# Performance work log

Hardware: AMD Instinct MI355X
Metric: run time of the kernel (lower is better)

Reference implementation:

```python
import jax, jax.numpy as jnp
import numpy as np

B, S, D, K = 8, 4096, 256, 8192
BETA = 0.25


def setup_inputs() -> dict:
    key = jax.random.key(0)
    k1, k2 = jax.random.split(key)
    return {
        "z": jax.random.normal(k1, (B, S, D), dtype=jnp.float32),
        "embed": jax.random.normal(k2, (K, D), dtype=jnp.float32),
    }


def reference(z, embed):
    # Inference-path VQ-EMA forward (EMA buffer updates are a no-grad side
    # effect only active in training mode; excluded from the pure reference).
    num_codes, dim = embed.shape
    z_flat = z.reshape(-1, dim)                      # [N, D]
    # squared-euclidean distances: ||z||^2 - 2 z.e^T + ||e||^2  -> [N, K]
    dist = ((z_flat * z_flat).sum(1, keepdims=True)
            - 2.0 * (z_flat @ embed.T)
            + (embed * embed).sum(1)[None, :])
    idx = jnp.argmin(dist, axis=1)                   # [N]
    z_q = embed[idx].reshape(z.shape)                # gather instead of onehot @ embed
    # commitment loss: beta * mse(stop_grad(z_q), z)
    loss = BETA * jnp.mean(jnp.square(jax.lax.stop_gradient(z_q) - z))
    # straight-through estimator
    z_q_st = z + jax.lax.stop_gradient(z_q - z)
    # perplexity from code usage histogram (scatter-add instead of onehot.mean)
    counts = jnp.zeros((num_codes,), dtype=z.dtype).at[idx].add(1.0)
    avg_probs = counts / idx.shape[0]
    perplexity = jnp.exp(-jnp.sum(avg_probs * jnp.log(avg_probs + 1e-12)))
    return z_q_st, loss, perplexity, idx.reshape(z.shape[:-1])
```

## Files before the change

kernel.cpp:

```cpp
#include <hip/hip_runtime.h>
#include <stdint.h>
#include <math.h>

#define NROWS 32768
#define DIM   256
#define KCODES 8192
#define BETA  0.25f
#define RSPLIT 16
#define NELEM 8388608
#define TAU 0.09375f

typedef float f32x4 __attribute__((ext_vector_type(4)));
typedef _Float16 v8h __attribute__((ext_vector_type(8)));
typedef unsigned short us4 __attribute__((ext_vector_type(4)));

__device__ inline unsigned int split1(float x) {
    _Float16 hf = (_Float16)x;
    _Float16 lf = (_Float16)(x - (float)hf);
    unsigned int h = __builtin_bit_cast(unsigned short, hf);
    unsigned int l = __builtin_bit_cast(unsigned short, lf);
    return h | (l << 16);
}

__device__ inline void gload_lds16(const void* g, void* l) {
    __builtin_amdgcn_global_load_lds(
        (const __attribute__((address_space(1))) void*)g,
        (__attribute__((address_space(3))) void*)l,
        16, 0, 0);
}

__device__ inline unsigned int fkey(float f) {
    unsigned int b = __float_as_uint(f);
    return (b & 0x80000000u) ? ~b : (b | 0x80000000u);
}

__global__ void prep_all(const float* __restrict__ z,
                         const float* __restrict__ e,
                         unsigned short* __restrict__ zhi,
                         unsigned short* __restrict__ zlo,
                         unsigned short* __restrict__ ehi,
                         unsigned short* __restrict__ elo,
                         float* __restrict__ enrm,
                         float* __restrict__ counts,
                         float* __restrict__ lossAcc,
                         int* __restrict__ flagcnt) {
    if (blockIdx.x < 8192) {
        int t = blockIdx.x * 256 + threadIdx.x;
        float4 v = reinterpret_cast<const float4*>(z)[t];
        unsigned int p0 = split1(v.x);
        unsigned int p1 = split1(v.y);
        unsigned int p2 = split1(v.z);
        unsigned int p3 = split1(v.w);
        us4 h, l;
        h[0] = (unsigned short)p0; l[0] = (unsigned short)(p0 >> 16);
        h[1] = (unsigned short)p1; l[1] = (unsigned short)(p1 >> 16);
        h[2] = (unsigned short)p2; l[2] = (unsigned short)(p2 >> 16);
        h[3] = (unsigned short)p3; l[3] = (unsigned short)(p3 >> 16);
        reinterpret_cast<us4*>(zhi)[t] = h;
        reinterpret_cast<us4*>(zlo)[t] = l;
    } else {
        int row = blockIdx.x - 8192;
        int d = threadIdx.x;
        float x = e[(size_t)row * DIM + d];
        unsigned int p = split1(x);
        ehi[(size_t)row * DIM + d] = (unsigned short)p;
        elo[(size_t)row * DIM + d] = (unsigned short)(p >> 16);
        float sq = x * x;
        #pragma unroll
        for (int off = 32; off; off >>= 1) sq += __shfl_down(sq, off);
        __shared__ float ps[4];
        if ((threadIdx.x & 63) == 0) ps[threadIdx.x >> 6] = sq;
        __syncthreads();
        if (threadIdx.x == 0) {
            enrm[row] = 0.5f * (ps[0] + ps[1] + ps[2] + ps[3]);
            counts[row] = 0.f;
            if (row == 0) { *lossAcc = 0.f; *flagcnt = 0; }
        }
    }
}

__launch_bounds__(512, 2)
__global__ void gemm_hi_fused(const unsigned short* __restrict__ zhi,
                              const unsigned short* __restrict__ ehi,
                              const float* __restrict__ enrm,
                              int* __restrict__ colidx,
                              float* __restrict__ out_idx,
                              int* __restrict__ flagcnt,
                              int* __restrict__ flaglist,
                              unsigned long long* __restrict__ rkey) {
    __shared__ __align__(16) unsigned short Bs[4][128 * 64];
    __shared__ float esL[KCODES];
    __shared__ float rvv[4][128];
    __shared__ float rv2s[4][128];
    __shared__ int   rcc[4][128];

    const int tid = threadIdx.x;
    const int w = tid >> 6, l = tid & 63;
    const int lx = l & 15, quad = l >> 4;
    const int wm = w >> 2, wn = w & 3;
    const int arow_base = blockIdx.x * 128;
    const int fr_lx7 = lx & 15 & 7;
    const int ecol = wn * 32 + lx;
    const int st_g = ((l & 7) ^ (l >> 3)) * 8;

    v8h af[4][8];
    #pragma unroll
    for (int mi = 0; mi < 4; ++mi) {
        const unsigned short* ap =
            zhi + (size_t)(arow_base + wm * 64 + mi * 16 + lx) * DIM + quad * 8;
        #pragma unroll
        for (int ks = 0; ks < 8; ++ks)
            af[mi][ks] = *(const v8h*)(ap + ks * 32);
    }

    #pragma unroll
    for (int j = 0; j < 4; ++j)
        gload_lds16(enrm + (j * 8 + w) * 256 + l * 4, &esL[(j * 8 + w) * 256]);

#define STAGE(BUF, NT, BK) do {                                               \
        const unsigned short* _s = ehi                                        \
            + (size_t)((NT) * 128 + (tid >> 3)) * DIM + (BK) * 64 + st_g;     \
        gload_lds16(_s,                    &Bs[BUF][(w * 8) * 64]);           \
        gload_lds16(_s + (size_t)64 * DIM, &Bs[BUF][(64 + w * 8) * 64]);      \
} while (0)

#define READF(DST, BUF) do {                                                  \
        _Pragma("unroll") for (int kc = 0; kc < 2; ++kc) {                    \
            const int gsw = ((kc * 4 + quad) ^ fr_lx7) * 8;                   \
            DST[kc * 2 + 0] = *(const v8h*)&Bs[BUF][(wn * 32 + lx) * 64 + gsw];      \
            DST[kc * 2 + 1] = *(const v8h*)&Bs[BUF][(wn * 32 + 16 + lx) * 64 + gsw]; \
        }                                                                     \
} while (0)

#define MFMAS(F, BK) do {                                                     \
        __builtin_amdgcn_s_setprio(1);                                        \
        _Pragma("unroll") for (int kc = 0; kc < 2; ++kc)                      \
            _Pragma("unroll") for (int mi = 0; mi < 4; ++mi) {                \
                acc[mi][0] = __builtin_amdgcn_mfma_f32_16x16x32_f16(          \
                    af[mi][(BK) * 2 + kc], F[kc * 2 + 0], acc[mi][0], 0, 0, 0); \
                acc[mi][1] = __builtin_amdgcn_mfma_f32_16x16x32_f16(          \
                    af[mi][(BK) * 2 + kc], F[kc * 2 + 1], acc[mi][1], 0, 0, 0); \
            }                                                                 \
        __builtin_amdgcn_s_setprio(0);                                        \
} while (0)

#define FENCE2 do {                                                           \
        asm volatile("s_waitcnt vmcnt(2)" ::: "memory");                      \
        __builtin_amdgcn_s_barrier();                                         \
        asm volatile("" ::: "memory");                                        \
} while (0)

#define EPILOGUE(NTV) do {                                                    \
        _Pragma("unroll") for (int ni = 0; ni < 2; ++ni) {                    \
            const int col = (NTV) * 128 + ecol + ni * 16;                     \
            _Pragma("unroll") for (int mi = 0; mi < 4; ++mi)                  \
                _Pragma("unroll") for (int r = 0; r < 4; ++r) {               \
                    const int s = mi * 4 + r;                                 \
                    const float a = acc[mi][ni][r];                           \
                    const bool gt = a > runm[s];                              \
                    runm2[s] = __builtin_amdgcn_fmed3f(a, runm[s], runm2[s]); \
                    runc[s] = gt ? col : runc[s];                             \
                    runm[s] = fmaxf(runm[s], a);                              \
                }                                                             \
        }                                                                     \
} while (0)

    STAGE(0, 0, 0);
    STAGE(1, 0, 1);
    v8h bA[4], bB[4];
    FENCE2;
    READF(bA, 0);
    float esn0 = esL[ecol];
    float esn1 = esL[ecol + 16];

    float runm[16], runm2[16];
    int runc[16];
    #pragma unroll
    for (int s = 0; s < 16; ++s) {
        runm[s] = -3.0e38f; runm2[s] = -3.0e38f; runc[s] = 0x7fffffff;
    }

    f32x4 acc[4][2];
    for (int nt = 0; nt < 64; ++nt) {
        const int ntn = (nt + 1) & 63;
        STAGE(2, nt, 2);
        FENCE2;
        {   const float a0 = -esn0, a1 = -esn1;
            #pragma unroll
            for (int mi = 0; mi < 4; ++mi) {
                acc[mi][0] = (f32x4){a0, a0, a0, a0};
                acc[mi][1] = (f32x4){a1, a1, a1, a1};
            }
        }
        READF(bB, 1);
        MFMAS(bA, 0);
        STAGE(3, nt, 3);
        FENCE2;
        READF(bA, 2);
        MFMAS(bB, 1);
        STAGE(0, ntn, 0);
        FENCE2;
        READF(bB, 3);
        MFMAS(bA, 2);
        STAGE(1, ntn, 1);
        FENCE2;
        READF(bA, 0);
        esn0 = esL[ntn * 128 + ecol];
        esn1 = esL[ntn * 128 + ecol + 16];
        MFMAS(bB, 3);
        EPILOGUE(nt);
    }
#undef STAGE
#undef READF
#undef MFMAS
#undef FENCE2
#undef EPILOGUE

    #pragma unroll
    for (int s = 0; s < 16; ++s) {
        float m1 = runm[s], m2 = runm2[s];
        int c1 = runc[s];
        #pragma unroll
        for (int m = 1; m < 16; m <<= 1) {
            float o1 = __shfl_xor(m1, m);
            int oc = __shfl_xor(c1, m);
            float o2 = __shfl_xor(m2, m);
            float mn = fminf(m1, o1);
            m2 = fmaxf(fmaxf(m2, o2), mn);
            bool take = (o1 > m1) || (o1 == m1 && oc < c1);
            m1 = take ? o1 : m1;
            c1 = take ? oc : c1;
        }
        if (lx == 0) {
            const int rl = wm * 64 + (s >> 2) * 16 + quad * 4 + (s & 3);
            rvv[wn][rl] = m1; rcc[wn][rl] = c1; rv2s[wn][rl] = m2;
        }
    }
    __syncthreads();
    if (tid < 128) {
        float m1 = rvv[0][tid], m2 = rv2s[0][tid];
        int c1 = rcc[0][tid];
        #pragma unroll
        for (int q = 1; q < 4; ++q) {
            float o1 = rvv[q][tid], o2 = rv2s[q][tid];
            int oc = rcc[q][tid];
            float mn = fminf(m1, o1);
            m2 = fmaxf(fmaxf(m2, o2), mn);
            bool take = (o1 > m1) || (o1 == m1 && oc < c1);
            m1 = take ? o1 : m1;
            c1 = take ? oc : c1;
        }
        const float v1 = -m1, v2 = -m2;
        const int row = arow_base + tid;
        out_idx[row] = (float)c1;
        if (v2 - v1 < TAU) {
            int slot = atomicAdd(flagcnt, 1);
            flaglist[slot] = row;
            rkey[slot] = ~0ull;
            colidx[row] = -(slot + 1);
        } else {
            colidx[row] = c1;
        }
    }
}

__launch_bounds__(256, 2)
__global__ void rescue_gemm(const unsigned short* __restrict__ zhi,
                            const unsigned short* __restrict__ zlo,
                            const unsigned short* __restrict__ ehi,
                            const unsigned short* __restrict__ elo,
                            const float* __restrict__ enrm,
                            const int* __restrict__ flagcnt,
                            const int* __restrict__ flaglist,
                            unsigned long long* __restrict__ rkey) {
    __shared__ __align__(16) unsigned short As[128 * 64];
    __shared__ __align__(16) unsigned short Bs[128 * 64];
    __shared__ float rv[2][128];
    __shared__ int   rc[2][128];

    const int count = *flagcnt;
    const int tid = threadIdx.x;
    const int w = tid >> 6, l = tid & 63;
    const int lx = l & 15, quad = l >> 4;
    const int wm = w >> 1, wn = w & 1;
    const int cs = blockIdx.y;
    const int cbase_cs = cs * (KCODES / RSPLIT);

    const int st_row8 = l >> 3;
    const int st_g = (((l & 7) ^ (l >> 3)) * 8);
    const int fr_lx7 = lx & 7;

    for (int tb = blockIdx.x * 128; tb < count; tb += 32 * 128) {
        int arowj[4];
        #pragma unroll
        for (int j = 0; j < 4; ++j) {
            int li = tb + w * 32 + j * 8 + st_row8;
            arowj[j] = (li < count) ? flaglist[li] : 0;
        }

        float runv[16];
        int runc[16];
        #pragma unroll
        for (int s = 0; s < 16; ++s) { runv[s] = 3.0e38f; runc[s] = 0x7fffffff; }

        for (int nt = 0; nt < (KCODES / RSPLIT) / 128; ++nt) {
            const int colbase = cbase_cs + nt * 128;
            f32x4 acc[4][4];
            #pragma unroll
            for (int mi = 0; mi < 4; ++mi)
                #pragma unroll
                for (int ni = 0; ni < 4; ++ni) {
                    f32x4 zz = {0.f, 0.f, 0.f, 0.f};
                    acc[mi][ni] = zz;
                }

            #pragma unroll
            for (int seg = 0; seg < 3; ++seg) {
                const unsigned short* za = (seg == 2) ? zlo : zhi;
                const unsigned short* eb = (seg == 1) ? elo : ehi;
                for (int bk = 0; bk < 4; ++bk) {
                    const int ao = bk * 64;
                    __syncthreads();
                    #pragma unroll
                    for (int j = 0; j < 4; ++j) {
                        const int r = w * 32 + j * 8 + st_row8;
                        gload_lds16(za + (size_t)arowj[j] * DIM + ao + st_g,
                                    &As[(w * 32 + j * 8) * 64]);
                        gload_lds16(eb + (size_t)(colbase + r) * DIM + ao + st_g,
                                    &Bs[(w * 32 + j * 8) * 64]);
                    }
                    __syncthreads();
                    #pragma unroll
                    for (int kc = 0; kc < 2; ++kc) {
                        const int gsw = ((kc * 4 + quad) ^ fr_lx7) * 8;
                        v8h af[4], bfr[4];
                        #pragma unroll
                        for (int mi = 0; mi < 4; ++mi)
                            af[mi] = *(const v8h*)&As[(wm * 64 + mi * 16 + lx) * 64 + gsw];
                        #pragma unroll
                        for (int ni = 0; ni < 4; ++ni)
                            bfr[ni] = *(const v8h*)&Bs[(wn * 64 + ni * 16 + lx) * 64 + gsw];
                        #pragma unroll
                        for (int mi = 0; mi < 4; ++mi)
                            #pragma unroll
                            for (int ni = 0; ni < 4; ++ni)
                                acc[mi][ni] = __builtin_amdgcn_mfma_f32_16x16x32_f16(
                                    af[mi], bfr[ni], acc[mi][ni], 0, 0, 0);
                    }
                }
            }

            #pragma unroll
            for (int ni = 0; ni < 4; ++ni) {
                const int col = colbase + wn * 64 + ni * 16 + lx;
                const float es = enrm[col];
                #pragma unroll
                for (int mi = 0; mi < 4; ++mi)
                    #pragma unroll
                    for (int r = 0; r < 4; ++r) {
                        float sv = es - acc[mi][ni][r];
                        const int s = mi * 4 + r;
                        if (sv < runv[s]) { runv[s] = sv; runc[s] = col; }
                    }
            }
        }

        #pragma unroll
        for (int s = 0; s < 16; ++s) {
            float v = runv[s]; int c = runc[s];
            #pragma unroll
            for (int m = 1; m < 16; m <<= 1) {
                float ov = __shfl_xor(v, m);
                int oc = __shfl_xor(c, m);
                if (ov < v || (ov == v && oc < c)) { v = ov; c = oc; }
            }
            if (lx == 0) {
                const int mi = s >> 2, r = s & 3;
                const int rl = wm * 64 + mi * 16 + quad * 4 + r;
                rv[wn][rl] = v; rc[wn][rl] = c;
            }
        }
        __syncthreads();
        if (tid < 128) {
            float v0 = rv[0][tid]; int c0 = rc[0][tid];
            float v1 = rv[1][tid]; int c1 = rc[1][tid];
            if (v1 < v0 || (v1 == v0 && c1 < c0)) { v0 = v1; c0 = c1; }
            const int li = tb + tid;
            if (li < count) {
                unsigned long long key =
                    ((unsigned long long)fkey(v0) << 32) | (unsigned int)c0;
                atomicMin(&rkey[li], key);
            }
        }
        __syncthreads();
    }
}

__global__ void fused_out(const int* __restrict__ colidx,
                          const unsigned long long* __restrict__ rkey,
                          const float* __restrict__ z,
                          const float* __restrict__ embed,
                          float* __restrict__ out_zq,
                          float* __restrict__ out_idx,
                          float* __restrict__ counts,
                          float* __restrict__ lossAcc) {
    __shared__ int cidx[16];
    const int tid = threadIdx.x;
    if (tid < 16) {
        const int row = blockIdx.x * 16 + tid;
        int c = colidx[row];
        if (c < 0) {
            c = (int)(unsigned int)(rkey[-c - 1] & 0x1FFFull);
            out_idx[row] = (float)c;
        }
        cidx[tid] = c;
        atomicAdd(&counts[c], 1.0f);
    }
    __syncthreads();
    const int d = tid;
    float ls = 0.f;
    #pragma unroll 4
    for (int i = 0; i < 16; ++i) {
        const int row = blockIdx.x * 16 + i;
        const int c = cidx[i];
        const float zv = z[(size_t)row * DIM + d];
        const float ev = embed[(size_t)c * DIM + d];
        const float diff = ev - zv;
        out_zq[(size_t)row * DIM + d] = zv + diff;
        ls += diff * diff;
    }
    #pragma unroll
    for (int off = 32; off; off >>= 1) ls += __shfl_down(ls, off);
    __shared__ float ps[4];
    if ((tid & 63) == 0) ps[tid >> 6] = ls;
    __syncthreads();
    if (tid == 0) atomicAdd(lossAcc, ps[0] + ps[1] + ps[2] + ps[3]);
}

__global__ void finalize(const float* __restrict__ counts,
                         const float* __restrict__ lossAcc,
                         float* __restrict__ out_loss,
                         float* __restrict__ out_perp) {
    float h = 0.f;
    for (int k = threadIdx.x; k < KCODES; k += 256) {
        float p = counts[k] * (1.0f / (float)NROWS);
        h += p * logf(p + 1e-12f);
    }
    #pragma unroll
    for (int off = 32; off; off >>= 1) h += __shfl_down(h, off);
    __shared__ float ps[4];
    if ((threadIdx.x & 63) == 0) ps[threadIdx.x >> 6] = h;
    __syncthreads();
    if (threadIdx.x == 0) {
        *out_perp = expf(-(ps[0] + ps[1] + ps[2] + ps[3]));
        *out_loss = BETA * lossAcc[0] / (float)NELEM;
    }
}

extern "C" void kernel_launch(void* const* d_in, const int* in_sizes, int n_in,
                              void* d_out, int out_size, void* d_ws, size_t ws_size,
                              hipStream_t stream) {
    const float* z = (const float*)d_in[0];
    const float* embed = (const float*)d_in[1];
    char* ws = (char*)d_ws;

    unsigned short* zhi = (unsigned short*)(ws + 0);
    unsigned short* zlo = (unsigned short*)(ws + 16777216);
    unsigned short* ehi = (unsigned short*)(ws + 33554432);
    unsigned short* elo = (unsigned short*)(ws + 37748736);
    float* enrm    = (float*)(ws + 41943040);
    int*   colidx  = (int*)  (ws + 43548672);
    float* counts  = (float*)(ws + 43679744);
    float* lossAcc = (float*)(ws + 43712512);
    int*   flagcnt = (int*)  (ws + 43712516);
    int*   flaglist = (int*) (ws + 43712520);
    unsigned long long* rkey = (unsigned long long*)(ws + 43843592);

    float* out = (float*)d_out;
    float* out_zq   = out;
    float* out_loss = out + 8388608;
    float* out_perp = out + 8388609;
    float* out_idx  = out + 8388610;

    prep_all<<<16384, 256, 0, stream>>>(z, embed, zhi, zlo, ehi, elo, enrm,
                                        counts, lossAcc, flagcnt);
    gemm_hi_fused<<<NROWS / 128, 512, 0, stream>>>(
        zhi, ehi, enrm, colidx, out_idx, flagcnt, flaglist, rkey);
    rescue_gemm<<<dim3(32, RSPLIT), 256, 0, stream>>>(
        zhi, zlo, ehi, elo, enrm, flagcnt, flaglist, rkey);
    fused_out<<<NROWS / 16, 256, 0, stream>>>(colidx, rkey, z, embed,
                                              out_zq, out_idx, counts, lossAcc);
    finalize<<<1, 256, 0, stream>>>(counts, lossAcc, out_loss, out_perp);
}
```

Before: 354.1 us.

## Shrink GEMM block to 64 rows with wider per-wave N tile and ping-pong accumulators

The fused distance GEMM now uses 256-thread blocks covering 64 rows, and each wave computes a 32x64 tile instead of 64x32. Two accumulator sets alternate so the argmin epilogue of one code tile overlaps the MFMAs of the next. Code norms are read straight from global memory instead of being staged into an LDS table. This halves the A-operand reuse per block and doubles the B-tile staging traffic per row computed, in exchange for more blocks, less LDS per block and hidden epilogue latency.

```diff
diff --git a/kernel.cpp b/kernel.cpp
--- a/kernel.cpp
+++ b/kernel.cpp
@@ -79,7 +79,7 @@
     }
 }
 
-__launch_bounds__(512, 2)
+__launch_bounds__(256, 2)
 __global__ void gemm_hi_fused(const unsigned short* __restrict__ zhi,
                               const unsigned short* __restrict__ ehi,
                               const float* __restrict__ enrm,
@@ -89,74 +89,92 @@
                               int* __restrict__ flaglist,
                               unsigned long long* __restrict__ rkey) {
     __shared__ __align__(16) unsigned short Bs[4][128 * 64];
-    __shared__ float esL[KCODES];
-    __shared__ float rvv[4][128];
-    __shared__ float rv2s[4][128];
-    __shared__ int   rcc[4][128];
+    __shared__ float rvv[2][64];
+    __shared__ float rv2s[2][64];
+    __shared__ int   rcc[2][64];
 
     const int tid = threadIdx.x;
     const int w = tid >> 6, l = tid & 63;
     const int lx = l & 15, quad = l >> 4;
-    const int wm = w >> 2, wn = w & 3;
-    const int arow_base = blockIdx.x * 128;
-    const int fr_lx7 = lx & 15 & 7;
-    const int ecol = wn * 32 + lx;
+    const int wm = w >> 1, wn = w & 1;
+    const int arow_base = blockIdx.x * 64;
+    const int fr = lx & 7;
+    const int ecol = wn * 64 + lx;
     const int st_g = ((l & 7) ^ (l >> 3)) * 8;
-
-    v8h af[4][8];
+    const int srow = tid >> 3;
+
+    v8h af[2][8];
     #pragma unroll
-    for (int mi = 0; mi < 4; ++mi) {
+    for (int mi = 0; mi < 2; ++mi) {
         const unsigned short* ap =
-            zhi + (size_t)(arow_base + wm * 64 + mi * 16 + lx) * DIM + quad * 8;
+            zhi + (size_t)(arow_base + wm * 32 + mi * 16 + lx) * DIM + quad * 8;
         #pragma unroll
         for (int ks = 0; ks < 8; ++ks)
             af[mi][ks] = *(const v8h*)(ap + ks * 32);
     }
 
-    #pragma unroll
-    for (int j = 0; j < 4; ++j)
-        gload_lds16(enrm + (j * 8 + w) * 256 + l * 4, &esL[(j * 8 + w) * 256]);
+    float esn0 = enrm[ecol];
+    float esn1 = enrm[ecol + 16];
+    float esn2 = enrm[ecol + 32];
+    float esn3 = enrm[ecol + 48];
 
 #define STAGE(BUF, NT, BK) do {                                               \
         const unsigned short* _s = ehi                                        \
-            + (size_t)((NT) * 128 + (tid >> 3)) * DIM + (BK) * 64 + st_g;     \
+            + (size_t)((NT) * 128 + srow) * DIM + (BK) * 64 + st_g;           \
         gload_lds16(_s,                    &Bs[BUF][(w * 8) * 64]);           \
+        gload_lds16(_s + (size_t)32 * DIM, &Bs[BUF][(32 + w * 8) * 64]);      \
         gload_lds16(_s + (size_t)64 * DIM, &Bs[BUF][(64 + w * 8) * 64]);      \
-} while (0)
-
-#define READF(DST, BUF) do {                                                  \
+        gload_lds16(_s + (size_t)96 * DIM, &Bs[BUF][(96 + w * 8) * 64]);      \
+} while (0)
+
+#define FENCE do {                                                            \
+        asm volatile("s_waitcnt vmcnt(8)" ::: "memory");                      \
+        __builtin_amdgcn_s_barrier();                                         \
+        asm volatile("" ::: "memory");                                        \
+} while (0)
+
+#define READF(BUF) do {                                                       \
         _Pragma("unroll") for (int kc = 0; kc < 2; ++kc) {                    \
-            const int gsw = ((kc * 4 + quad) ^ fr_lx7) * 8;                   \
-            DST[kc * 2 + 0] = *(const v8h*)&Bs[BUF][(wn * 32 + lx) * 64 + gsw];      \
-            DST[kc * 2 + 1] = *(const v8h*)&Bs[BUF][(wn * 32 + 16 + lx) * 64 + gsw]; \
+            const int gsw = ((kc * 4 + quad) ^ fr) * 8;                       \
+            _Pragma("unroll") for (int ni = 0; ni < 4; ++ni)                  \
+                bf[kc * 4 + ni] =                                             \
+                    *(const v8h*)&Bs[BUF][(wn * 64 + ni * 16 + lx) * 64 + gsw]; \
         }                                                                     \
 } while (0)
 
-#define MFMAS(F, BK) do {                                                     \
+#define MFMAS(ACC, BK) do {                                                   \
         __builtin_amdgcn_s_setprio(1);                                        \
         _Pragma("unroll") for (int kc = 0; kc < 2; ++kc)                      \
-            _Pragma("unroll") for (int mi = 0; mi < 4; ++mi) {                \
-                acc[mi][0] = __builtin_amdgcn_mfma_f32_16x16x32_f16(          \
-                    af[mi][(BK) * 2 + kc], F[kc * 2 + 0], acc[mi][0], 0, 0, 0); \
-                acc[mi][1] = __builtin_amdgcn_mfma_f32_16x16x32_f16(          \
-                    af[mi][(BK) * 2 + kc], F[kc * 2 + 1], acc[mi][1], 0, 0, 0); \
-            }                                                                 \
+            _Pragma("unroll") for (int mi = 0; mi < 2; ++mi)                  \
+                _Pragma("unroll") for (int ni = 0; ni < 4; ++ni)              \
+                    ACC[mi][ni] = __builtin_amdgcn_mfma_f32_16x16x32_f16(     \
+                        af[mi][(BK) * 2 + kc], bf[kc * 4 + ni],               \
+                        ACC[mi][ni], 0, 0, 0);                                \
         __builtin_amdgcn_s_setprio(0);                                        \
 } while (0)
 
-#define FENCE2 do {                                                           \
-        asm volatile("s_waitcnt vmcnt(2)" ::: "memory");                      \
-        __builtin_amdgcn_s_barrier();                                         \
-        asm volatile("" ::: "memory");                                        \
-} while (0)
-
-#define EPILOGUE(NTV) do {                                                    \
-        _Pragma("unroll") for (int ni = 0; ni < 2; ++ni) {                    \
+#define INITACC(ACC) do {                                                     \
+        _Pragma("unroll") for (int mi = 0; mi < 2; ++mi) {                    \
+            ACC[mi][0] = (f32x4){-esn0, -esn0, -esn0, -esn0};                 \
+            ACC[mi][1] = (f32x4){-esn1, -esn1, -esn1, -esn1};                 \
+            ACC[mi][2] = (f32x4){-esn2, -esn2, -esn2, -esn2};                 \
+            ACC[mi][3] = (f32x4){-esn3, -esn3, -esn3, -esn3};                 \
+        }                                                                     \
+} while (0)
+
+#define ESLOAD(NT) do {                                                       \
+        const int _b = (NT) * 128 + ecol;                                     \
+        esn0 = enrm[_b]; esn1 = enrm[_b + 16];                                \
+        esn2 = enrm[_b + 32]; esn3 = enrm[_b + 48];                           \
+} while (0)
+
+#define EPILOGUE(ACC, NTV) do {                                               \
+        _Pragma("unroll") for (int ni = 0; ni < 4; ++ni) {                    \
             const int col = (NTV) * 128 + ecol + ni * 16;                     \
-            _Pragma("unroll") for (int mi = 0; mi < 4; ++mi)                  \
+            _Pragma("unroll") for (int mi = 0; mi < 2; ++mi)                  \
                 _Pragma("unroll") for (int r = 0; r < 4; ++r) {               \
                     const int s = mi * 4 + r;                                 \
-                    const float a = acc[mi][ni][r];                           \
+                    const float a = ACC[mi][ni][r];                           \
                     const bool gt = a > runm[s];                              \
                     runm2[s] = __builtin_amdgcn_fmed3f(a, runm[s], runm2[s]); \
                     runc[s] = gt ? col : runc[s];                             \
@@ -165,59 +183,49 @@
         }                                                                     \
 } while (0)
 
+    float runm[8], runm2[8];
+    int runc[8];
+    #pragma unroll
+    for (int s = 0; s < 8; ++s) {
+        runm[s] = -3.0e38f; runm2[s] = -3.0e38f; runc[s] = 0x7fffffff;
+    }
+
+    f32x4 accA[2][4], accB[2][4];
+    #pragma unroll
+    for (int mi = 0; mi < 2; ++mi)
+        #pragma unroll
+        for (int ni = 0; ni < 4; ++ni)
+            accB[mi][ni] = (f32x4){-3.0e38f, -3.0e38f, -3.0e38f, -3.0e38f};
+
+    v8h bf[8];
     STAGE(0, 0, 0);
     STAGE(1, 0, 1);
-    v8h bA[4], bB[4];
-    FENCE2;
-    READF(bA, 0);
-    float esn0 = esL[ecol];
-    float esn1 = esL[ecol + 16];
-
-    float runm[16], runm2[16];
-    int runc[16];
-    #pragma unroll
-    for (int s = 0; s < 16; ++s) {
-        runm[s] = -3.0e38f; runm2[s] = -3.0e38f; runc[s] = 0x7fffffff;
-    }
-
-    f32x4 acc[4][2];
-    for (int nt = 0; nt < 64; ++nt) {
-        const int ntn = (nt + 1) & 63;
-        STAGE(2, nt, 2);
-        FENCE2;
-        {   const float a0 = -esn0, a1 = -esn1;
-            #pragma unroll
-            for (int mi = 0; mi < 4; ++mi) {
-                acc[mi][0] = (f32x4){a0, a0, a0, a0};
-                acc[mi][1] = (f32x4){a1, a1, a1, a1};
-            }
-        }
-        READF(bB, 1);
-        MFMAS(bA, 0);
-        STAGE(3, nt, 3);
-        FENCE2;
-        READF(bA, 2);
-        MFMAS(bB, 1);
-        STAGE(0, ntn, 0);
-        FENCE2;
-        READF(bB, 3);
-        MFMAS(bA, 2);
-        STAGE(1, ntn, 1);
-        FENCE2;
-        READF(bA, 0);
-        esn0 = esL[ntn * 128 + ecol];
-        esn1 = esL[ntn * 128 + ecol + 16];
-        MFMAS(bB, 3);
-        EPILOGUE(nt);
-    }
+
+    for (int nt2 = 0; nt2 < 32; ++nt2) {
+        const int ntA = nt2 * 2, ntB = ntA + 1;
+        const int ntC = (ntB + 1) & 63;
+        STAGE(2, ntA, 2); FENCE; READF(0);
+        INITACC(accA); MFMAS(accA, 0); EPILOGUE(accB, ntA - 1);
+        ESLOAD(ntB);      STAGE(3, ntA, 3); FENCE; READF(1); MFMAS(accA, 1);
+        STAGE(0, ntB, 0); FENCE; READF(2); MFMAS(accA, 2);
+        STAGE(1, ntB, 1); FENCE; READF(3); MFMAS(accA, 3);
+        STAGE(2, ntB, 2); FENCE; READF(0);
+        INITACC(accB); MFMAS(accB, 0); EPILOGUE(accA, ntA);
+        ESLOAD(ntC);      STAGE(3, ntB, 3); FENCE; READF(1); MFMAS(accB, 1);
+        STAGE(0, ntC, 0); FENCE; READF(2); MFMAS(accB, 2);
+        STAGE(1, ntC, 1); FENCE; READF(3); MFMAS(accB, 3);
+    }
+    EPILOGUE(accB, 63);
 #undef STAGE
+#undef FENCE
 #undef READF
 #undef MFMAS
-#undef FENCE2
+#undef INITACC
+#undef ESLOAD
 #undef EPILOGUE
 
     #pragma unroll
-    for (int s = 0; s < 16; ++s) {
+    for (int s = 0; s < 8; ++s) {
         float m1 = runm[s], m2 = runm2[s];
         int c1 = runc[s];
         #pragma unroll
@@ -232,18 +240,17 @@
             c1 = take ? oc : c1;
         }
         if (lx == 0) {
-            const int rl = wm * 64 + (s >> 2) * 16 + quad * 4 + (s & 3);
+            const int rl = wm * 32 + (s >> 2) * 16 + quad * 4 + (s & 3);
             rvv[wn][rl] = m1; rcc[wn][rl] = c1; rv2s[wn][rl] = m2;
         }
     }
     __syncthreads();
-    if (tid < 128) {
+    if (tid < 64) {
         float m1 = rvv[0][tid], m2 = rv2s[0][tid];
         int c1 = rcc[0][tid];
-        #pragma unroll
-        for (int q = 1; q < 4; ++q) {
-            float o1 = rvv[q][tid], o2 = rv2s[q][tid];
-            int oc = rcc[q][tid];
+        {
+            float o1 = rvv[1][tid], o2 = rv2s[1][tid];
+            int oc = rcc[1][tid];
             float mn = fminf(m1, o1);
             m2 = fmaxf(fmaxf(m2, o2), mn);
             bool take = (o1 > m1) || (o1 == m1 && oc < c1);
@@ -484,7 +491,7 @@
 
     prep_all<<<16384, 256, 0, stream>>>(z, embed, zhi, zlo, ehi, elo, enrm,
                                         counts, lossAcc, flagcnt);
-    gemm_hi_fused<<<NROWS / 128, 512, 0, stream>>>(
+    gemm_hi_fused<<<NROWS / 64, 256, 0, stream>>>(
         zhi, ehi, enrm, colidx, out_idx, flagcnt, flaglist, rkey);
     rescue_gemm<<<dim3(32, RSPLIT), 256, 0, stream>>>(
         zhi, zlo, ehi, elo, enrm, flagcnt, flaglist, rkey);
```

Result: faster. 345.7 us (-2.4%).
